# Kernel tuning notes

Hardware: AMD Instinct MI355X
Metric: run time of the kernel (lower is better)

The kernel has to match this reference:

```python
import jax, jax.numpy as jnp
import numpy as np

N = 50000      # nodes
E = 800000     # edges (before self loops)
D_IN = 64      # input atom feature dim
HID = 128      # hidden_dim
HEADS = 4
C = HID // HEADS  # 32 per-head channels
ED = 12        # edge feature dim
L = 4          # num GAT layers
EPS = 1e-5


def setup_inputs() -> dict:
    key = jax.random.key(0)
    ks = jax.random.split(key, 10)
    s = 0.1
    return {
        "x": jax.random.normal(ks[0], (N, D_IN), jnp.float32),
        "edge_index": jax.random.randint(ks[1], (2, E), 0, N, dtype=jnp.int32),
        "edge_attr": jax.random.uniform(ks[2], (E, ED), jnp.float32),
        "Wp": jax.random.normal(ks[3], (D_IN, HID), jnp.float32) * s,
        "bp": jnp.zeros((HID,), jnp.float32),
        "W": jax.random.normal(ks[4], (L, HID, HID), jnp.float32) * s,
        "We": jax.random.normal(ks[5], (L, ED, HID), jnp.float32) * s,
        "att_src": jax.random.normal(ks[6], (L, HEADS, C), jnp.float32) * s,
        "att_dst": jax.random.normal(ks[7], (L, HEADS, C), jnp.float32) * s,
        "att_edge": jax.random.normal(ks[8], (L, HEADS, C), jnp.float32) * s,
        "bias": jnp.zeros((L, HID), jnp.float32),
        "gamma": jnp.ones((L, HID), jnp.float32),
        "beta": jnp.zeros((L, HID), jnp.float32),
    }


def _gat_layer(h, src, dst, ea_full, W, We, a_s, a_d, a_e, b):
    # PyG GATConv: x' = x W -> [N, heads, C]; attention uses edge features, msg = alpha * x'_src
    xp = (h @ W).reshape(N, HEADS, C)
    e_emb = (ea_full @ We).reshape(-1, HEADS, C)          # [E', heads, C]
    a_src = (xp * a_s).sum(-1)                            # [N, heads]
    a_dst = (xp * a_d).sum(-1)
    a = a_src[src] + a_dst[dst] + (e_emb * a_e).sum(-1)   # [E', heads]
    a = jax.nn.leaky_relu(a, 0.2)
    # segment softmax over destination node neighborhoods
    amax = jax.ops.segment_max(a, dst, num_segments=N)
    ex = jnp.exp(a - amax[dst])
    denom = jax.ops.segment_sum(ex, dst, num_segments=N)
    alpha = ex / denom[dst]                               # [E', heads]
    msg = alpha[:, :, None] * xp[src]                     # [E', heads, C]
    out = jax.ops.segment_sum(msg, dst, num_segments=N)   # [N, heads, C]
    return out.reshape(N, HID) + b


def reference(x, edge_index, edge_attr, Wp, bp, W, We, att_src, att_dst, att_edge, bias, gamma, beta):
    # PyG GATConv add_self_loops=True with fill_value='mean' for edge_attr
    loop = jnp.arange(N, dtype=edge_index.dtype)
    src = jnp.concatenate([edge_index[0], loop])
    dst = jnp.concatenate([edge_index[1], loop])
    ea_mean = edge_attr.mean(0)
    ea_full = jnp.concatenate([edge_attr, jnp.broadcast_to(ea_mean, (N, ED))], 0)

    h = jax.nn.relu(x @ Wp + bp)
    for i in range(L):
        h_in = h
        h = _gat_layer(h, src, dst, ea_full, W[i], We[i], att_src[i], att_dst[i], att_edge[i], bias[i])
        # BatchNorm1d (training-mode batch statistics)
        mu = h.mean(0)
        var = ((h - mu) ** 2).mean(0)
        h = gamma[i] * (h - mu) / jnp.sqrt(var + EPS) + beta[i]
        h = jax.nn.relu(h)
        if i > 0:
            h = h + h_in
    return h
```

## Files before the change

kernel.cpp:

```cpp
#include <hip/hip_runtime.h>

constexpr int N_NODES = 50000;
constexpr int N_EDGES = 800000;
constexpr int N_ETOT  = N_EDGES + N_NODES;
constexpr int HID     = 128;
constexpr int HEADS   = 4;
constexpr int ED      = 12;
constexpr int LAYERS  = 4;
constexpr float BN_EPS = 1e-5f;
constexpr int EB = (N_ETOT + 255) / 256;
constexpr int GB = (N_NODES + 63) / 64;
constexpr int WB = (LAYERS * HID * HID + 255) / 256;
constexpr int CHUNK  = 2048;
constexpr int NCHUNK = (N_ETOT + CHUNK - 1) / CHUNK;
constexpr int NB     = (N_NODES + 127) / 128;
constexpr int F_TOT  = NB * NCHUNK;
constexpr int SB3    = (F_TOT + 255) / 256;

typedef __attribute__((ext_vector_type(8))) short short8;
typedef __attribute__((ext_vector_type(4))) float floatx4;

__device__ inline unsigned bf16pair(float a, float b) {
    unsigned ua = __float_as_uint(a), ub = __float_as_uint(b);
    ua = (ua + 0x7FFFu + ((ua >> 16) & 1u)) >> 16;
    ub = (ub + 0x7FFFu + ((ub >> 16) & 1u)) >> 16;
    return ua | (ub << 16);
}

__launch_bounds__(256)
__global__ void pre1_kernel(const int* __restrict__ dst, int* __restrict__ counts,
                            const float* __restrict__ ea, float* __restrict__ easum,
                            const float* __restrict__ W, unsigned short* __restrict__ wb,
                            const float* __restrict__ A, const float* __restrict__ B,
                            const float* __restrict__ bias, float* __restrict__ C,
                            unsigned* __restrict__ Cb) {
    __shared__ float smem[64 * 128];
    int bid = blockIdx.x, t = threadIdx.x;
    if (bid < GB) {
        constexpr int K = 64;
        const float4* B4 = (const float4*)B;
        float4* Bs4 = (float4*)smem;
#pragma unroll
        for (int i = t; i < K * 32; i += 256) Bs4[i] = B4[i];
        __syncthreads();

        int c0 = (t & 15) * 8;
        int r0 = (t >> 4) * 4;
        int rbase = bid * 64 + r0;

        float acc[4][8];
#pragma unroll
        for (int j = 0; j < 4; j++)
#pragma unroll
            for (int c = 0; c < 8; c++) acc[j][c] = 0.f;

        const float4* A4 = (const float4*)A;
        int rg[4];
#pragma unroll
        for (int j = 0; j < 4; j++) rg[j] = min(rbase + j, N_NODES - 1);

        for (int kk = 0; kk < K; kk += 4) {
            float4 av[4];
#pragma unroll
            for (int j = 0; j < 4; j++) av[j] = A4[(size_t)rg[j] * (K / 4) + (kk >> 2)];
            float a_arr[4][4];
#pragma unroll
            for (int j = 0; j < 4; j++) {
                a_arr[j][0] = av[j].x; a_arr[j][1] = av[j].y;
                a_arr[j][2] = av[j].z; a_arr[j][3] = av[j].w;
            }
#pragma unroll
            for (int jj = 0; jj < 4; jj++) {
                float4 b0 = Bs4[(kk + jj) * 32 + (c0 >> 2)];
                float4 b1 = Bs4[(kk + jj) * 32 + (c0 >> 2) + 1];
#pragma unroll
                for (int j = 0; j < 4; j++) {
                    float a = a_arr[j][jj];
                    acc[j][0] += a * b0.x; acc[j][1] += a * b0.y;
                    acc[j][2] += a * b0.z; acc[j][3] += a * b0.w;
                    acc[j][4] += a * b1.x; acc[j][5] += a * b1.y;
                    acc[j][6] += a * b1.z; acc[j][7] += a * b1.w;
                }
            }
        }

#pragma unroll
        for (int j = 0; j < 4; j++) {
            int r = rbase + j;
            if (r < N_NODES) {
                float o[8];
#pragma unroll
                for (int c = 0; c < 8; c++) o[c] = fmaxf(acc[j][c] + bias[c0 + c], 0.f);
                ((float4*)(C + (size_t)r * 128 + c0))[0] = make_float4(o[0], o[1], o[2], o[3]);
                ((float4*)(C + (size_t)r * 128 + c0 + 4))[0] = make_float4(o[4], o[5], o[6], o[7]);
                uint4 pk;
                pk.x = bf16pair(o[0], o[1]); pk.y = bf16pair(o[2], o[3]);
                pk.z = bf16pair(o[4], o[5]); pk.w = bf16pair(o[6], o[7]);
                ((uint4*)(Cb + (size_t)r * 64 + (c0 >> 1)))[0] = pk;
            }
        }
    } else if (bid < GB + NCHUNK) {
        int chunk = bid - GB;
        int* lh = (int*)smem;
        for (int i = t; i < NB; i += 256) lh[i] = 0;
        __syncthreads();
        int e0 = chunk * CHUNK;
        int eend = min(e0 + CHUNK, N_ETOT);
        for (int e = e0 + t; e < eend; e += 256) {
            int d = (e < N_EDGES) ? dst[e] : (e - N_EDGES);
            atomicAdd(&lh[d >> 7], 1);
        }
        __syncthreads();
        for (int i = t; i < NB; i += 256) counts[(size_t)chunk * NB + i] = lh[i];
    } else if (bid < GB + NCHUNK + 256) {
        int b2 = bid - GB - NCHUNK;
        float* ls = smem;
        if (t < 12) ls[t] = 0.f;
        __syncthreads();
        float loc[12];
#pragma unroll
        for (int d = 0; d < 12; d++) loc[d] = 0.f;
        for (int e = b2 * 256 + t; e < N_EDGES; e += 256 * 256) {
            const float* er = ea + (size_t)e * ED;
#pragma unroll
            for (int d = 0; d < 12; d++) loc[d] += er[d];
        }
#pragma unroll
        for (int d = 0; d < 12; d++) atomicAdd(&ls[d], loc[d]);
        __syncthreads();
        if (t < 12) atomicAdd(&easum[t], ls[t]);
    } else {
        int idx = (bid - GB - NCHUNK - 256) * 256 + t;
        if (idx < LAYERS * HID * HID) {
            int l = idx >> 14;
            int k = (idx >> 7) & 127;
            int n = idx & 127;
            unsigned u = __float_as_uint(W[idx]);
            u = (u + 0x7FFFu + ((u >> 16) & 1u)) >> 16;
            int kt = k >> 5, q = (k & 31) >> 3, j = k & 7;
            int nt = n >> 4, c = n & 15;
            int lane = q * 16 + c;
            wb[(size_t)l * 16384 + ((size_t)(kt * 8 + nt) * 64 + lane) * 8 + j] =
                (unsigned short)u;
        }
    }
}

__global__ void blocksum2_kernel(const int* __restrict__ counts, int* __restrict__ bsum) {
    __shared__ int sd[256];
    int t = threadIdx.x;
    int j = blockIdx.x * 256 + t;
    int v = 0;
    if (j < F_TOT) {
        int bb = j / NCHUNK, cc = j - bb * NCHUNK;
        v = counts[(size_t)cc * NB + bb];
    }
    sd[t] = v;
    __syncthreads();
#pragma unroll
    for (int off = 128; off; off >>= 1) {
        if (t < off) sd[t] += sd[t + off];
        __syncthreads();
    }
    if (t == 0) bsum[blockIdx.x] = sd[0];
}

__launch_bounds__(256)
__global__ void pre2_kernel(const int* __restrict__ bsum, int* __restrict__ boff,
                            int* __restrict__ chunkbase, int* __restrict__ rowp,
                            const float* __restrict__ easum,
                            const float* __restrict__ We, const float* __restrict__ att_edge,
                            float* __restrict__ wea_all, float* __restrict__ aloop) {
    int t = threadIdx.x;
    if (blockIdx.x == 0) {
        __shared__ int sd[256];
        int b = 3 * t;
        int v0 = (b + 0 < SB3) ? bsum[b + 0] : 0;
        int v1 = (b + 1 < SB3) ? bsum[b + 1] : 0;
        int v2 = (b + 2 < SB3) ? bsum[b + 2] : 0;
        int tot = v0 + v1 + v2;
        sd[t] = tot;
        __syncthreads();
#pragma unroll
        for (int off = 1; off < 256; off <<= 1) {
            int u = (t >= off) ? sd[t - off] : 0;
            __syncthreads();
            sd[t] += u;
            __syncthreads();
        }
        int excl = sd[t] - tot;
        if (b + 0 < SB3) boff[b + 0] = excl;
        if (b + 1 < SB3) boff[b + 1] = excl + v0;
        if (b + 2 < SB3) boff[b + 2] = excl + v0 + v1;
        if (t == 255) {
            chunkbase[F_TOT] = sd[255];
            rowp[N_NODES] = N_ETOT;
        }
    } else {
        __shared__ float em[12];
        __shared__ float weash[LAYERS * ED * HEADS];
        if (t < 12) em[t] = easum[t] / (float)N_EDGES;
        if (t < LAYERS * ED * HEADS) {
            int l = t / (ED * HEADS);
            int r = t % (ED * HEADS);
            int d = r / HEADS;
            int h = r % HEADS;
            float sum = 0.f;
#pragma unroll
            for (int c = 0; c < 32; c++)
                sum += We[((size_t)(l * ED + d)) * HID + h * 32 + c] *
                       att_edge[(l * HEADS + h) * 32 + c];
            wea_all[t] = sum;
            weash[t] = sum;
        }
        __syncthreads();
        if (t < LAYERS * HEADS) {
            int l = t / HEADS, h = t % HEADS;
            float s = 0.f;
#pragma unroll
            for (int d = 0; d < 12; d++) s += em[d] * weash[l * ED * HEADS + d * HEADS + h];
            aloop[t] = s;
        }
    }
}

__global__ void addback_kernel(const int* __restrict__ counts, const int* __restrict__ boff,
                               int* __restrict__ chunkbase) {
    __shared__ int sd[256];
    int t = threadIdx.x;
    int j = blockIdx.x * 256 + t;
    int v = 0;
    if (j < F_TOT) {
        int bb = j / NCHUNK, cc = j - bb * NCHUNK;
        v = counts[(size_t)cc * NB + bb];
    }
    sd[t] = v;
    __syncthreads();
#pragma unroll
    for (int off = 1; off < 256; off <<= 1) {
        int u = (t >= off) ? sd[t - off] : 0;
        __syncthreads();
        sd[t] += u;
        __syncthreads();
    }
    if (j < F_TOT) chunkbase[j] = sd[t] - v + boff[blockIdx.x];
}

__launch_bounds__(256)
__global__ void pre3_kernel(const unsigned short* __restrict__ hAb,
                            const unsigned short* __restrict__ wb,
                            const float* __restrict__ att_s, const float* __restrict__ att_d,
                            unsigned* __restrict__ xpb,
                            float* __restrict__ asrc, float* __restrict__ adst,
                            const int* __restrict__ src, const int* __restrict__ dst,
                            const int* __restrict__ chunkbase, int2* __restrict__ bucketed) {
    __shared__ float smem[4 * 16 * 129];
    int t = threadIdx.x;
    if (blockIdx.x >= GB) {
        int chunk = blockIdx.x - GB;
        int* lb = (int*)smem;
        int* lh = lb + NB;
        for (int i = t; i < NB; i += 256) {
            lb[i] = chunkbase[(size_t)i * NCHUNK + chunk];
            lh[i] = 0;
        }
        __syncthreads();
        int e0 = chunk * CHUNK;
        int eend = min(e0 + CHUNK, N_ETOT);
        for (int e = e0 + t; e < eend; e += 256) {
            int s, d;
            if (e < N_EDGES) { s = src[e]; d = dst[e]; }
            else             { s = d = e - N_EDGES; }
            int b = d >> 7;
            int lr = atomicAdd(&lh[b], 1);
            bucketed[lb[b] + lr] = make_int2(s, e | ((d & 127) << 20));
        }
        return;
    }
    int bid = blockIdx.x;
    float (*lds)[16][129] = (float (*)[16][129])smem;
    int w = t >> 6, lane = t & 63;
    int rbase = bid * 64 + w * 16;
    int mrow = lane & 15, quad = lane >> 4;

    floatx4 acc[8];
#pragma unroll
    for (int nt = 0; nt < 8; nt++) acc[nt] = (floatx4){0.f, 0.f, 0.f, 0.f};

    int arow = min(rbase + mrow, N_NODES - 1);
    const short8* wb8 = (const short8*)wb;
#pragma unroll
    for (int kt = 0; kt < 4; kt++) {
        short8 afrag = *(const short8*)(hAb + (size_t)arow * 128 + kt * 32 + quad * 8);
#pragma unroll
        for (int nt = 0; nt < 8; nt++) {
            short8 bfrag = wb8[(kt * 8 + nt) * 64 + lane];
            acc[nt] = __builtin_amdgcn_mfma_f32_16x16x32_bf16(afrag, bfrag, acc[nt], 0, 0, 0);
        }
    }
#pragma unroll
    for (int nt = 0; nt < 8; nt++)
#pragma unroll
        for (int rr = 0; rr < 4; rr++)
            lds[w][quad * 4 + rr][nt * 16 + mrow] = acc[nt][rr];

    int row = lane >> 2, h = lane & 3;
    int r = rbase + row;
    float vals[32];
    float ps = 0.f, pd = 0.f;
#pragma unroll
    for (int c = 0; c < 32; c++) {
        float v = lds[w][row][h * 32 + c];
        vals[c] = v;
        ps += v * att_s[h * 32 + c];
        pd += v * att_d[h * 32 + c];
    }
    if (r < N_NODES) {
        unsigned* dstp = xpb + (size_t)r * 64 + h * 16;
#pragma unroll
        for (int qq = 0; qq < 4; qq++) {
            uint4 o;
            o.x = bf16pair(vals[qq * 8 + 0], vals[qq * 8 + 1]);
            o.y = bf16pair(vals[qq * 8 + 2], vals[qq * 8 + 3]);
            o.z = bf16pair(vals[qq * 8 + 4], vals[qq * 8 + 5]);
            o.w = bf16pair(vals[qq * 8 + 6], vals[qq * 8 + 7]);
            ((uint4*)dstp)[qq] = o;
        }
        asrc[r * 4 + h] = ps;
        adst[r * 4 + h] = pd;
    }
}

__launch_bounds__(256)
__global__ void csrd_kernel(const int2* __restrict__ bucketed, const int* __restrict__ chunkbase,
                            int2* __restrict__ csr, int* __restrict__ rowp) {
    __shared__ int hist[128], exc[128], cur[128];
    int b = blockIdx.x, t = threadIdx.x;
    int base = chunkbase[(size_t)b * NCHUNK];
    int cend = chunkbase[(size_t)(b + 1) * NCHUNK];
    int cnt = cend - base;
    if (t < 128) { hist[t] = 0; cur[t] = 0; }
    __syncthreads();
    for (int i = t; i < cnt; i += 256)
        atomicAdd(&hist[(bucketed[base + i].y >> 20) & 127], 1);
    __syncthreads();
    if (t < 128) exc[t] = hist[t];
    __syncthreads();
#pragma unroll
    for (int off = 1; off < 128; off <<= 1) {
        int u = (t < 128 && t >= off) ? exc[t - off] : 0;
        __syncthreads();
        if (t < 128) exc[t] += u;
        __syncthreads();
    }
    if (t < 128) {
        exc[t] -= hist[t];
        int node = b * 128 + t;
        if (node < N_NODES) rowp[node] = base + exc[t];
    }
    __syncthreads();
    for (int i = t; i < cnt; i += 256) {
        int2 r = bucketed[base + i];
        int dl = (r.y >> 20) & 127;
        int lr = atomicAdd(&cur[dl], 1);
        csr[base + exc[dl] + lr] = make_int2(r.x, r.y & 0xFFFFF);
    }
}

__launch_bounds__(256)
__global__ void pre4_kernel(const int2* __restrict__ csr, const float* __restrict__ ea,
                            const float* __restrict__ wea_all, const float* __restrict__ aloop,
                            uint2* __restrict__ aecsr) {
    __shared__ float wsh[LAYERS * ED * HEADS];
    __shared__ float lsh[LAYERS * HEADS];
    int t = threadIdx.x;
    if (t < LAYERS * ED * HEADS) wsh[t] = wea_all[t];
    if (t < LAYERS * HEADS) lsh[t] = aloop[t];
    __syncthreads();
    int i = blockIdx.x * 256 + t;
    if (i >= N_ETOT) return;
    int e = csr[i].y;
    float a[LAYERS][4];
    if (e < N_EDGES) {
        float er[12];
        const float* ep = ea + (size_t)e * ED;
#pragma unroll
        for (int d = 0; d < 12; d++) er[d] = ep[d];
#pragma unroll
        for (int l = 0; l < LAYERS; l++)
#pragma unroll
            for (int h = 0; h < 4; h++) {
                float s = 0.f;
#pragma unroll
                for (int d = 0; d < 12; d++) s += er[d] * wsh[l * 48 + d * 4 + h];
                a[l][h] = s;
            }
    } else {
#pragma unroll
        for (int l = 0; l < LAYERS; l++)
#pragma unroll
            for (int h = 0; h < 4; h++) a[l][h] = lsh[l * 4 + h];
    }
#pragma unroll
    for (int l = 0; l < LAYERS; l++)
        aecsr[(size_t)l * N_ETOT + i] =
            make_uint2(bf16pair(a[l][0], a[l][1]), bf16pair(a[l][2], a[l][3]));
}

template <int ADD>
__launch_bounds__(256)
__global__ void gemm_fused_kernel(const float* __restrict__ outb,
                                  const float* __restrict__ bnsum,
                                  const float* __restrict__ bnsum2,
                                  const float* __restrict__ gamma,
                                  const float* __restrict__ beta,
                                  float* __restrict__ hA,
                                  const unsigned short* __restrict__ wb,
                                  const float* __restrict__ att_s,
                                  const float* __restrict__ att_d,
                                  unsigned* __restrict__ xpb,
                                  float* __restrict__ asrc, float* __restrict__ adst) {
    __shared__ float lds[4][16][129];
    __shared__ float sc_s[128], sh_s[128];
    int t = threadIdx.x;
    if (t < 128) {
        float mu = bnsum[t] / (float)N_NODES;
        float var = bnsum2[t] / (float)N_NODES - mu * mu;
        float inv = rsqrtf(var + BN_EPS);
        float g = gamma[t] * inv;
        sc_s[t] = g;
        sh_s[t] = beta[t] - mu * g;
    }
    __syncthreads();

    int w = t >> 6, lane = t & 63;
    int rbase = blockIdx.x * 64 + w * 16;
    int mrow = lane & 15, quad = lane >> 4;
    int arow = rbase + mrow;
    bool owner = arow < N_NODES;
    int ar = min(arow, N_NODES - 1);

    floatx4 acc[8];
#pragma unroll
    for (int nt = 0; nt < 8; nt++) acc[nt] = (floatx4){0.f, 0.f, 0.f, 0.f};

    const short8* wb8 = (const short8*)wb;
#pragma unroll
    for (int kt = 0; kt < 4; kt++) {
        int cb = kt * 32 + quad * 8;
        const float4* ob = (const float4*)(outb + (size_t)ar * 128 + cb);
        float4 o0 = ob[0], o1 = ob[1];
        float v[8];
        v[0] = fmaxf(o0.x * sc_s[cb + 0] + sh_s[cb + 0], 0.f);
        v[1] = fmaxf(o0.y * sc_s[cb + 1] + sh_s[cb + 1], 0.f);
        v[2] = fmaxf(o0.z * sc_s[cb + 2] + sh_s[cb + 2], 0.f);
        v[3] = fmaxf(o0.w * sc_s[cb + 3] + sh_s[cb + 3], 0.f);
        v[4] = fmaxf(o1.x * sc_s[cb + 4] + sh_s[cb + 4], 0.f);
        v[5] = fmaxf(o1.y * sc_s[cb + 5] + sh_s[cb + 5], 0.f);
        v[6] = fmaxf(o1.z * sc_s[cb + 6] + sh_s[cb + 6], 0.f);
        v[7] = fmaxf(o1.w * sc_s[cb + 7] + sh_s[cb + 7], 0.f);
        if (ADD) {
            const float4* hp = (const float4*)(hA + (size_t)ar * 128 + cb);
            float4 h0 = hp[0], h1 = hp[1];
            v[0] += h0.x; v[1] += h0.y; v[2] += h0.z; v[3] += h0.w;
            v[4] += h1.x; v[5] += h1.y; v[6] += h1.z; v[7] += h1.w;
        }
        if (owner) {
            float4* hw = (float4*)(hA + (size_t)ar * 128 + cb);
            hw[0] = make_float4(v[0], v[1], v[2], v[3]);
            hw[1] = make_float4(v[4], v[5], v[6], v[7]);
        }
        uint4 pk;
        pk.x = bf16pair(v[0], v[1]); pk.y = bf16pair(v[2], v[3]);
        pk.z = bf16pair(v[4], v[5]); pk.w = bf16pair(v[6], v[7]);
        short8 afrag = *(short8*)&pk;
#pragma unroll
        for (int nt = 0; nt < 8; nt++) {
            short8 bfrag = wb8[(kt * 8 + nt) * 64 + lane];
            acc[nt] = __builtin_amdgcn_mfma_f32_16x16x32_bf16(afrag, bfrag, acc[nt], 0, 0, 0);
        }
    }

#pragma unroll
    for (int nt = 0; nt < 8; nt++)
#pragma unroll
        for (int rr = 0; rr < 4; rr++)
            lds[w][quad * 4 + rr][nt * 16 + mrow] = acc[nt][rr];

    int row = lane >> 2, h = lane & 3;
    int r = rbase + row;
    float vals[32];
    float ps = 0.f, pd = 0.f;
#pragma unroll
    for (int c = 0; c < 32; c++) {
        float v = lds[w][row][h * 32 + c];
        vals[c] = v;
        ps += v * att_s[h * 32 + c];
        pd += v * att_d[h * 32 + c];
    }
    if (r < N_NODES) {
        unsigned* dstp = xpb + (size_t)r * 64 + h * 16;
#pragma unroll
        for (int qq = 0; qq < 4; qq++) {
            uint4 o;
            o.x = bf16pair(vals[qq * 8 + 0], vals[qq * 8 + 1]);
            o.y = bf16pair(vals[qq * 8 + 2], vals[qq * 8 + 3]);
            o.z = bf16pair(vals[qq * 8 + 4], vals[qq * 8 + 5]);
            o.w = bf16pair(vals[qq * 8 + 6], vals[qq * 8 + 7]);
            ((uint4*)dstp)[qq] = o;
        }
        asrc[r * 4 + h] = ps;
        adst[r * 4 + h] = pd;
    }
}

__launch_bounds__(256)
__global__ void node_kernel(const uint2* __restrict__ aecsr, const float* __restrict__ asrc,
                            const float* __restrict__ adst, const int* __restrict__ rowp,
                            const int2* __restrict__ csr, const unsigned* __restrict__ xpb,
                            float* __restrict__ out) {
    int gw = (blockIdx.x * blockDim.x + threadIdx.x) >> 6;
    int lane = threadIdx.x & 63;
    if (gw >= N_NODES) return;
    int sub = lane >> 4;
    int sl  = lane & 15;
    int h   = sl >> 2;
    int beg = rowp[gw], end = rowp[gw + 1];
    const uint4* xp4 = (const uint4*)xpb;
    float adh = adst[gw * 4 + h];

    float a[8];
#pragma unroll
    for (int c = 0; c < 8; c++) a[c] = 0.f;
    float den = 0.f;

#define PROC(JJ)                                                                 \
    {                                                                            \
        int2 se = csr[JJ];                                                       \
        uint2 ae = aecsr[JJ];                                                    \
        unsigned aw = (h & 2) ? ae.y : ae.x;                                     \
        float aeh = __uint_as_float((h & 1) ? (aw & 0xFFFF0000u) : (aw << 16));  \
        float ash = asrc[se.x * 4 + h];                                          \
        uint4 v = xp4[(size_t)se.x * 16 + sl];                                   \
        float lg = ash + adh + aeh;                                              \
        lg = (lg > 0.f) ? lg : 0.2f * lg;                                        \
        float ex = __expf(fminf(lg, 60.f));                                      \
        a[0] += ex * __uint_as_float(v.x << 16);                                 \
        a[1] += ex * __uint_as_float(v.x & 0xFFFF0000u);                         \
        a[2] += ex * __uint_as_float(v.y << 16);                                 \
        a[3] += ex * __uint_as_float(v.y & 0xFFFF0000u);                         \
        a[4] += ex * __uint_as_float(v.z << 16);                                 \
        a[5] += ex * __uint_as_float(v.z & 0xFFFF0000u);                         \
        a[6] += ex * __uint_as_float(v.w << 16);                                 \
        a[7] += ex * __uint_as_float(v.w & 0xFFFF0000u);                         \
        den += ex;                                                               \
    }

    int j = beg + sub;
    for (; j + 12 < end; j += 16) {
        PROC(j); PROC(j + 4); PROC(j + 8); PROC(j + 12);
    }
    for (; j < end; j += 4) PROC(j);
#undef PROC

#pragma unroll
    for (int c = 0; c < 8; c++) {
        a[c] += __shfl_xor(a[c], 16);
        a[c] += __shfl_xor(a[c], 32);
    }
    den += __shfl_xor(den, 16);
    den += __shfl_xor(den, 32);
    float inv = 1.0f / den;
    if (sub == 0) {
        float* op = out + (size_t)gw * 128 + sl * 8;
        ((float4*)op)[0] = make_float4(a[0] * inv, a[1] * inv, a[2] * inv, a[3] * inv);
        ((float4*)op)[1] = make_float4(a[4] * inv, a[5] * inv, a[6] * inv, a[7] * inv);
    }
}

__launch_bounds__(256)
__global__ void bnstats_kernel(const float* __restrict__ h, float* __restrict__ bnsum,
                               float* __restrict__ bnsum2) {
    __shared__ float ls[256], ls2[256];
    int t = threadIdx.x;
    int c = t & 127, half = t >> 7;
    int r0 = blockIdx.x * 128;
    float s = 0.f, s2 = 0.f;
    int rend = min(r0 + 128, N_NODES);
    for (int r = r0 + half; r < rend; r += 2) {
        float v = h[(size_t)r * 128 + c];
        s += v; s2 += v * v;
    }
    ls[t] = s; ls2[t] = s2;
    __syncthreads();
    if (half == 0) {
        s += ls[t + 128]; s2 += ls2[t + 128];
        atomicAdd(&bnsum[c], s);
        atomicAdd(&bnsum2[c], s2);
    }
}

__launch_bounds__(256)
__global__ void finalupd_kernel(const float* __restrict__ outb, const float* __restrict__ bnsum,
                                const float* __restrict__ bnsum2, const float* __restrict__ gamma,
                                const float* __restrict__ beta, const float* __restrict__ hA,
                                float* __restrict__ dst) {
    __shared__ float sc_s[128], sh_s[128];
    int t = threadIdx.x;
    if (t < 128) {
        float mu = bnsum[t] / (float)N_NODES;
        float var = bnsum2[t] / (float)N_NODES - mu * mu;
        float inv = rsqrtf(var + BN_EPS);
        float g = gamma[t] * inv;
        sc_s[t] = g;
        sh_s[t] = beta[t] - mu * g;
    }
    __syncthreads();
    int i = blockIdx.x * blockDim.x + t;
    if (i >= N_NODES * 32) return;
    int c4 = (i & 31) * 4;
    float4 o = ((const float4*)outb)[i];
    float4 hh = ((const float4*)hA)[i];
    float4 v;
    v.x = fmaxf(o.x * sc_s[c4 + 0] + sh_s[c4 + 0], 0.f) + hh.x;
    v.y = fmaxf(o.y * sc_s[c4 + 1] + sh_s[c4 + 1], 0.f) + hh.y;
    v.z = fmaxf(o.z * sc_s[c4 + 2] + sh_s[c4 + 2], 0.f) + hh.z;
    v.w = fmaxf(o.w * sc_s[c4 + 3] + sh_s[c4 + 3], 0.f) + hh.w;
    ((float4*)dst)[i] = v;
}

extern "C" void kernel_launch(void* const* d_in, const int* in_sizes, int n_in,
                              void* d_out, int out_size, void* d_ws, size_t ws_size,
                              hipStream_t stream) {
    const float* x          = (const float*)d_in[0];
    const int*   edge_index = (const int*)d_in[1];
    const float* edge_attr  = (const float*)d_in[2];
    const float* Wp         = (const float*)d_in[3];
    const float* bp         = (const float*)d_in[4];
    const float* W          = (const float*)d_in[5];
    const float* We         = (const float*)d_in[6];
    const float* att_src    = (const float*)d_in[7];
    const float* att_dst    = (const float*)d_in[8];
    const float* att_edge   = (const float*)d_in[9];
    const float* gamma      = (const float*)d_in[11];
    const float* beta       = (const float*)d_in[12];
    float* outp = (float*)d_out;

    const int* ei_src = edge_index;
    const int* ei_dst = edge_index + N_EDGES;

    char* p = (char*)d_ws;
    auto alloc = [&](size_t nbytes) {
        char* r = p;
        p += (nbytes + 255) & ~(size_t)255;
        return r;
    };
    float* easum    = (float*)alloc(16 * 4);
    float* bnsumall = (float*)alloc((size_t)LAYERS * 256 * 4);
    size_t zero_bytes = (char*)(bnsumall + LAYERS * 256) - (char*)easum;

    float* hA       = (float*)alloc((size_t)N_NODES * 128 * 4);
    unsigned* hAb   = (unsigned*)alloc((size_t)N_NODES * 64 * 4);
    unsigned* xpb   = (unsigned*)alloc((size_t)N_NODES * 64 * 4);
    float* outb     = (float*)alloc((size_t)N_NODES * 128 * 4);
    float* asrc     = (float*)alloc((size_t)N_NODES * 4 * 4);
    float* adst     = (float*)alloc((size_t)N_NODES * 4 * 4);
    float* wea_all  = (float*)alloc((LAYERS * 48 + 16) * 4);
    float* aloop    = wea_all + LAYERS * 48;
    unsigned short* wb = (unsigned short*)alloc((size_t)LAYERS * 16384 * 2);
    int* rowp       = (int*)alloc(((size_t)N_NODES + 1) * 4);
    int* counts     = (int*)alloc((size_t)F_TOT * 4);
    int* chunkbase  = (int*)alloc(((size_t)F_TOT + 1) * 4);
    int2* bucketed  = (int2*)alloc((size_t)N_ETOT * 8);
    int2* csr       = (int2*)alloc((size_t)N_ETOT * 8);
    uint2* aecsr    = (uint2*)alloc((size_t)LAYERS * N_ETOT * 8);
    int* bsum       = (int*)alloc(1024 * 4);
    int* boff       = (int*)alloc(1024 * 4);

    (void)hipMemsetAsync(easum, 0, zero_bytes, stream);

    pre1_kernel<<<GB + NCHUNK + 256 + WB, 256, 0, stream>>>(
        ei_dst, counts, edge_attr, easum, W, wb, x, Wp, bp, hA, hAb);
    blocksum2_kernel<<<SB3, 256, 0, stream>>>(counts, bsum);
    pre2_kernel<<<2, 256, 0, stream>>>(bsum, boff, chunkbase, rowp, easum, We, att_edge,
                                       wea_all, aloop);
    addback_kernel<<<SB3, 256, 0, stream>>>(counts, boff, chunkbase);
    pre3_kernel<<<GB + NCHUNK, 256, 0, stream>>>(
        (const unsigned short*)hAb, wb, att_src, att_dst, xpb, asrc, adst,
        ei_src, ei_dst, chunkbase, bucketed);
    csrd_kernel<<<NB, 256, 0, stream>>>(bucketed, chunkbase, csr, rowp);
    pre4_kernel<<<EB, 256, 0, stream>>>(csr, edge_attr, wea_all, aloop, aecsr);

    for (int l = 0; l < LAYERS; l++) {
        float* bnsum  = bnsumall + l * 256;
        float* bnsum2 = bnsum + 128;
        node_kernel<<<(N_NODES + 3) / 4, 256, 0, stream>>>(
            aecsr + (size_t)l * N_ETOT, asrc, adst, rowp, csr, xpb, outb);
        bnstats_kernel<<<(N_NODES + 127) / 128, 256, 0, stream>>>(outb, bnsum, bnsum2);
        if (l < LAYERS - 1) {
            if (l == 0)
                gemm_fused_kernel<0><<<GB, 256, 0, stream>>>(
                    outb, bnsum, bnsum2, gamma + l * 128, beta + l * 128, hA,
                    wb + (size_t)(l + 1) * 16384, att_src + (l + 1) * 128,
                    att_dst + (l + 1) * 128, xpb, asrc, adst);
            else
                gemm_fused_kernel<1><<<GB, 256, 0, stream>>>(
                    outb, bnsum, bnsum2, gamma + l * 128, beta + l * 128, hA,
                    wb + (size_t)(l + 1) * 16384, att_src + (l + 1) * 128,
                    att_dst + (l + 1) * 128, xpb, asrc, adst);
        } else {
            finalupd_kernel<<<(N_NODES * 32 + 255) / 256, 256, 0, stream>>>(
                outb, bnsum, bnsum2, gamma + l * 128, beta + l * 128, hA, outp);
        }
    }
}
```

Measured before the change: 569.5 us.

## Store projected features head-major and process heads sequentially in node kernel

```diff
diff --git a/kernel.cpp b/kernel.cpp
--- a/kernel.cpp
+++ b/kernel.cpp
@@ -11,6 +11,7 @@
 constexpr int EB = (N_ETOT + 255) / 256;
 constexpr int GB = (N_NODES + 63) / 64;
 constexpr int WB = (LAYERS * HID * HID + 255) / 256;
+constexpr int NODE_BLKS = (N_NODES + 3) / 4;
 constexpr int CHUNK  = 2048;
 constexpr int NCHUNK = (N_ETOT + CHUNK - 1) / CHUNK;
 constexpr int NB     = (N_NODES + 127) / 128;
@@ -316,7 +317,7 @@
         pd += v * att_d[h * 32 + c];
     }
     if (r < N_NODES) {
-        unsigned* dstp = xpb + (size_t)r * 64 + h * 16;
+        unsigned* dstp = xpb + (size_t)h * N_NODES * 16 + (size_t)r * 16;
 #pragma unroll
         for (int qq = 0; qq < 4; qq++) {
             uint4 o;
@@ -499,7 +500,7 @@
         pd += v * att_d[h * 32 + c];
     }
     if (r < N_NODES) {
-        unsigned* dstp = xpb + (size_t)r * 64 + h * 16;
+        unsigned* dstp = xpb + (size_t)h * N_NODES * 16 + (size_t)r * 16;
 #pragma unroll
         for (int qq = 0; qq < 4; qq++) {
             uint4 o;
@@ -522,59 +523,47 @@
     int gw = (blockIdx.x * blockDim.x + threadIdx.x) >> 6;
     int lane = threadIdx.x & 63;
     if (gw >= N_NODES) return;
-    int sub = lane >> 4;
-    int sl  = lane & 15;
-    int h   = sl >> 2;
+    int sub = lane >> 3;
+    int sl  = lane & 7;
     int beg = rowp[gw], end = rowp[gw + 1];
-    const uint4* xp4 = (const uint4*)xpb;
-    float adh = adst[gw * 4 + h];
-
-    float a[8];
-#pragma unroll
-    for (int c = 0; c < 8; c++) a[c] = 0.f;
-    float den = 0.f;
-
-#define PROC(JJ)                                                                 \
-    {                                                                            \
-        int2 se = csr[JJ];                                                       \
-        uint2 ae = aecsr[JJ];                                                    \
-        unsigned aw = (h & 2) ? ae.y : ae.x;                                     \
-        float aeh = __uint_as_float((h & 1) ? (aw & 0xFFFF0000u) : (aw << 16));  \
-        float ash = asrc[se.x * 4 + h];                                          \
-        uint4 v = xp4[(size_t)se.x * 16 + sl];                                   \
-        float lg = ash + adh + aeh;                                              \
-        lg = (lg > 0.f) ? lg : 0.2f * lg;                                        \
-        float ex = __expf(fminf(lg, 60.f));                                      \
-        a[0] += ex * __uint_as_float(v.x << 16);                                 \
-        a[1] += ex * __uint_as_float(v.x & 0xFFFF0000u);                         \
-        a[2] += ex * __uint_as_float(v.y << 16);                                 \
-        a[3] += ex * __uint_as_float(v.y & 0xFFFF0000u);                         \
-        a[4] += ex * __uint_as_float(v.z << 16);                                 \
-        a[5] += ex * __uint_as_float(v.z & 0xFFFF0000u);                         \
-        a[6] += ex * __uint_as_float(v.w << 16);                                 \
-        a[7] += ex * __uint_as_float(v.w & 0xFFFF0000u);                         \
-        den += ex;                                                               \
-    }
-
-    int j = beg + sub;
-    for (; j + 12 < end; j += 16) {
-        PROC(j); PROC(j + 4); PROC(j + 8); PROC(j + 12);
-    }
-    for (; j < end; j += 4) PROC(j);
-#undef PROC
-
-#pragma unroll
-    for (int c = 0; c < 8; c++) {
-        a[c] += __shfl_xor(a[c], 16);
-        a[c] += __shfl_xor(a[c], 32);
-    }
-    den += __shfl_xor(den, 16);
-    den += __shfl_xor(den, 32);
-    float inv = 1.0f / den;
-    if (sub == 0) {
-        float* op = out + (size_t)gw * 128 + sl * 8;
-        ((float4*)op)[0] = make_float4(a[0] * inv, a[1] * inv, a[2] * inv, a[3] * inv);
-        ((float4*)op)[1] = make_float4(a[4] * inv, a[5] * inv, a[6] * inv, a[7] * inv);
+    const uint2* xp2 = (const uint2*)xpb;
+
+#pragma unroll
+    for (int h = 0; h < 4; h++) {
+        float adh = adst[gw * 4 + h];
+        const uint2* xph = xp2 + (size_t)h * N_NODES * 8;
+        float a0 = 0.f, a1 = 0.f, a2 = 0.f, a3 = 0.f;
+        float den = 0.f;
+        for (int j = beg + sub; j < end; j += 8) {
+            int2 se = csr[j];
+            uint2 ae = aecsr[j];
+            unsigned aw = (h & 2) ? ae.y : ae.x;
+            float aeh = __uint_as_float((h & 1) ? (aw & 0xFFFF0000u) : (aw << 16));
+            float ash = asrc[se.x * 4 + h];
+            uint2 v = xph[(size_t)se.x * 8 + sl];
+            float lg = ash + adh + aeh;
+            lg = (lg > 0.f) ? lg : 0.2f * lg;
+            float ex = __expf(fminf(lg, 60.f));
+            a0 += ex * __uint_as_float(v.x << 16);
+            a1 += ex * __uint_as_float(v.x & 0xFFFF0000u);
+            a2 += ex * __uint_as_float(v.y << 16);
+            a3 += ex * __uint_as_float(v.y & 0xFFFF0000u);
+            den += ex;
+        }
+        a0 += __shfl_xor(a0, 8);  a1 += __shfl_xor(a1, 8);
+        a2 += __shfl_xor(a2, 8);  a3 += __shfl_xor(a3, 8);
+        den += __shfl_xor(den, 8);
+        a0 += __shfl_xor(a0, 16); a1 += __shfl_xor(a1, 16);
+        a2 += __shfl_xor(a2, 16); a3 += __shfl_xor(a3, 16);
+        den += __shfl_xor(den, 16);
+        a0 += __shfl_xor(a0, 32); a1 += __shfl_xor(a1, 32);
+        a2 += __shfl_xor(a2, 32); a3 += __shfl_xor(a3, 32);
+        den += __shfl_xor(den, 32);
+        float inv = 1.0f / den;
+        if (sub == 0) {
+            float* op = out + (size_t)gw * 128 + h * 32 + sl * 4;
+            ((float4*)op)[0] = make_float4(a0 * inv, a1 * inv, a2 * inv, a3 * inv);
+        }
     }
 }
 
@@ -694,7 +683,7 @@
     for (int l = 0; l < LAYERS; l++) {
         float* bnsum  = bnsumall + l * 256;
         float* bnsum2 = bnsum + 128;
-        node_kernel<<<(N_NODES + 3) / 4, 256, 0, stream>>>(
+        node_kernel<<<NODE_BLKS, 256, 0, stream>>>(
             aecsr + (size_t)l * N_ETOT, asrc, adst, rowp, csr, xpb, outb);
         bnstats_kernel<<<(N_NODES + 127) / 128, 256, 0, stream>>>(outb, bnsum, bnsum2);
         if (l < LAYERS - 1) {
```

Measured after the change: 708.8 us. 1.24x slower.
